# Optimization experiments

Hardware: AMD Instinct MI355X
Metric: run time of the kernel (lower is better)

Reference implementation:

```python
import jax, jax.numpy as jnp
import numpy as np

NT, NP, E, H, DIM = 100000, 50000, 800000, 128, 128


def _lin(key, fi, fo):
    k1, k2 = jax.random.split(key)
    w = jax.random.normal(k1, (fi, fo), jnp.float32) * 0.02
    b = jax.random.normal(k2, (fo,), jnp.float32) * 0.02
    return w, b


def _conv_params(key, d_src, d_dst, d_out):
    ks = jax.random.split(key, 5)
    Wq, bq = _lin(ks[0], d_dst, d_out)
    Wk, bk = _lin(ks[1], d_src, d_out)
    Wv, bv = _lin(ks[2], d_src, d_out)
    Ws, bs = _lin(ks[3], d_dst, d_out)
    Wb = jax.random.normal(ks[4], (3 * d_out, 1), jnp.float32) * 0.02
    return Wq, bq, Wk, bk, Wv, bv, Ws, bs, Wb


def setup_inputs() -> dict:
    key = jax.random.key(0)
    ks = jax.random.split(key, 12)
    inp = {}
    inp['x_token'] = jax.random.normal(ks[0], (NT, 1), jnp.float32)
    inp['x_phrase'] = jax.random.normal(ks[1], (NP, H), jnp.float32)
    inp['W_emb'], inp['b_emb'] = _lin(ks[2], 1, H)
    (inp['Wq_tp'], inp['bq_tp'], inp['Wk_tp'], inp['bk_tp'], inp['Wv_tp'],
     inp['bv_tp'], inp['Ws_tp'], inp['bs_tp'], inp['Wb_tp']) = _conv_params(ks[3], H, H, H)
    (inp['Wq_pt'], inp['bq_pt'], inp['Wk_pt'], inp['bk_pt'], inp['Wv_pt'],
     inp['bv_pt'], inp['Ws_pt'], inp['bs_pt'], inp['Wb_pt']) = _conv_params(ks[4], H, H, H)
    inp['W_head'], inp['b_head'] = _lin(ks[5], H, DIM)
    inp['src_tp'] = jax.random.randint(ks[6], (E,), 0, NT, jnp.int32)
    inp['dst_tp'] = jax.random.randint(ks[7], (E,), 0, NP, jnp.int32)
    inp['src_pt'] = jax.random.randint(ks[8], (E,), 0, NP, jnp.int32)
    inp['dst_pt'] = jax.random.randint(ks[9], (E,), 0, NT, jnp.int32)
    return inp


def _tconv(x_src, x_dst, src, dst, Wq, bq, Wk, bk, Wv, bv, Ws, bs, Wb):
    # PyG TransformerConv, heads=1, beta=True, eval mode (no dropout).
    n_dst = x_dst.shape[0]
    d = Wq.shape[1]
    q = x_dst @ Wq + bq          # [Ndst, d]
    k = x_src @ Wk + bk          # [Nsrc, d]
    v = x_src @ Wv + bv          # [Nsrc, d]
    scores = jnp.sum(q[dst] * k[src], axis=-1) / jnp.sqrt(jnp.float32(d))  # [E]
    m = jax.ops.segment_max(scores, dst, num_segments=n_dst)
    m = jnp.where(jnp.isfinite(m), m, 0.0)  # nodes with no in-edges
    e = jnp.exp(scores - m[dst])
    denom = jax.ops.segment_sum(e, dst, num_segments=n_dst)
    alpha = e / (denom[dst] + 1e-16)                       # segment softmax over dst
    out = jax.ops.segment_sum(alpha[:, None] * v[src], dst, num_segments=n_dst)
    skip = x_dst @ Ws + bs
    beta = jax.nn.sigmoid(jnp.concatenate([out, skip, out - skip], axis=-1) @ Wb)
    return beta * skip + (1.0 - beta) * out


def _forward(x_token, x_phrase, W_emb, b_emb,
             Wq_tp, bq_tp, Wk_tp, bk_tp, Wv_tp, bv_tp, Ws_tp, bs_tp, Wb_tp,
             Wq_pt, bq_pt, Wk_pt, bk_pt, Wv_pt, bv_pt, Ws_pt, bs_pt, Wb_pt,
             W_head, b_head, src_tp, dst_tp, src_pt, dst_pt):
    h_t = x_token @ W_emb + b_emb   # [NT, H]
    h_p = x_phrase                  # [NP, H]
    # conv1 (HeteroConv aggr='sum'; each node type has exactly one incoming edge type)
    p1 = _tconv(h_t, h_p, src_tp, dst_tp, Wq_tp, bq_tp, Wk_tp, bk_tp, Wv_tp, bv_tp, Ws_tp, bs_tp, Wb_tp)
    t1 = _tconv(h_p, h_t, src_pt, dst_pt, Wq_pt, bq_pt, Wk_pt, bk_pt, Wv_pt, bv_pt, Ws_pt, bs_pt, Wb_pt)
    p1 = jax.nn.leaky_relu(p1, 0.01)
    t1 = jax.nn.leaky_relu(t1, 0.01)
    # conv2 shares the SAME conv modules (same params). Only the token output is used downstream.
    t2 = _tconv(p1, t1, src_pt, dst_pt, Wq_pt, bq_pt, Wk_pt, bk_pt, Wv_pt, bv_pt, Ws_pt, bs_pt, Wb_pt)
    return t2 @ W_head + b_head     # [NT, DIM]


def reference(x_token, x_phrase, W_emb, b_emb, Wq_tp, bq_tp, Wk_tp, bk_tp, Wv_tp, bv_tp, Ws_tp, bs_tp, Wb_tp, Wq_pt, bq_pt, Wk_pt, bk_pt, Wv_pt, bv_pt, Ws_pt, bs_pt, Wb_pt, W_head, b_head, src_tp, dst_tp, src_pt, dst_pt):
    return _forward(x_token, x_phrase, W_emb, b_emb,
                    Wq_tp, bq_tp, Wk_tp, bk_tp, Wv_tp, bv_tp, Ws_tp, bs_tp, Wb_tp,
                    Wq_pt, bq_pt, Wk_pt, bk_pt, Wv_pt, bv_pt, Ws_pt, bs_pt, Wb_pt,
                    W_head, b_head, src_tp, dst_tp, src_pt, dst_pt)
```

## Files before the change

### kernel.cpp

```cpp
#include <hip/hip_runtime.h>
#include <math.h>

#define NT 100000
#define NP 50000
#define NE 800000
#define H 128
#define NB 196
#define BCAP 8192
#define SPAD 140

#define CDIV(a,b) (((a)+(b)-1)/(b))

typedef __attribute__((ext_vector_type(8))) short s16x8;
typedef __attribute__((ext_vector_type(4))) short s16x4;
typedef __attribute__((ext_vector_type(4))) unsigned short u16x4;
typedef __attribute__((ext_vector_type(4))) float f32x4;

static __device__ __forceinline__ float dot4(float4 a, float4 b){
  return a.x*b.x + a.y*b.y + a.z*b.z + a.w*b.w;
}
static __device__ __forceinline__ float b2f(unsigned short u){
  union { unsigned int i; float f; } c; c.i = ((unsigned int)u) << 16; return c.f;
}
static __device__ __forceinline__ unsigned short f2b(float f){
  union { float f; unsigned int i; } c; c.f = f;
  unsigned int x = c.i;
  unsigned int r = (x + 0x7fffu + ((x >> 16) & 1u)) >> 16;
  return (unsigned short)r;
}
static __device__ __forceinline__ float4 cvt4u(u16x4 h){
  return make_float4(b2f(h[0]), b2f(h[1]), b2f(h[2]), b2f(h[3]));
}

__global__ void kvec4(const float* __restrict__ e, const float* __restrict__ be,
    const float* W0, const float* bi0, float* u0, float* w0,
    const float* W1, const float* bi1, float* u1, float* w1,
    const float* W2, const float* bi2, float* u2, float* w2,
    const float* W3, const float* bi3, float* u3, float* w3){
  const float *W, *bi; float *u, *w;
  switch (blockIdx.x){
    case 0: W=W0; bi=bi0; u=u0; w=w0; break;
    case 1: W=W1; bi=bi1; u=u1; w=w1; break;
    case 2: W=W2; bi=bi2; u=u2; w=w2; break;
    default:W=W3; bi=bi3; u=u3; w=w3; break;
  }
  int j = threadIdx.x;
  float su = 0.f, sw = 0.f;
  for (int i = 0; i < H; ++i) {
    float wv = W[i*H + j];
    su += e[i]*wv;
    sw += be[i]*wv;
  }
  u[j] = su;
  w[j] = sw + bi[j];
}

__global__ void ksetup(const float* __restrict__ Wq, const float* __restrict__ Wk,
                       const float* __restrict__ bq, float* __restrict__ Wqk,
                       float* __restrict__ bqk){
  int i = blockIdx.x;
  int m = threadIdx.x;
  __shared__ float wqr[H];
  wqr[m] = Wq[i*H + m];
  __syncthreads();
  const float* wkr = Wk + m*H;
  float s = 0.f;
  for (int j = 0; j < H; ++j) s += wqr[j] * wkr[j];
  Wqk[i*H + m] = s;
  if (i == 0){
    float t = 0.f;
    for (int j = 0; j < H; ++j) t += bq[j] * wkr[j];
    bqk[m] = t;
  }
}
__global__ void kvqb(const float* __restrict__ Wq, const float* __restrict__ bq,
                     const float* __restrict__ bk, float* __restrict__ vqb,
                     float* __restrict__ c0){
  int i = threadIdx.x;
  float s = 0.f;
  for (int j = 0; j < H; ++j) s += Wq[i*H + j]*bk[j];
  vqb[i] = s;
  if (i == 0){
    float t = 0.f;
    for (int j = 0; j < H; ++j) t += bq[j]*bk[j];
    *c0 = t;
  }
}

__global__ void kprep(const float* W0, unsigned short* P0,
                      const float* W1, unsigned short* P1,
                      const float* W2, unsigned short* P2,
                      const float* W3, unsigned short* P3,
                      const float* W4, unsigned short* P4,
                      const float* W5, unsigned short* P5,
                      const float* W6, unsigned short* P6){
  const float* W; unsigned short* P;
  switch (blockIdx.x){
    case 0: W=W0; P=P0; break;
    case 1: W=W1; P=P1; break;
    case 2: W=W2; P=P2; break;
    case 3: W=W3; P=P3; break;
    case 4: W=W4; P=P4; break;
    case 5: W=W5; P=P5; break;
    default:W=W6; P=P6; break;
  }
  int tid = threadIdx.x;
  for (int it = 0; it < 16; ++it){
    int gid = it*256 + tid;
    int n  = gid & 127;
    int kg = gid >> 7;
    int k0 = kg*4;
    float w0 = W[(k0+0)*H + n];
    float w1 = W[(k0+1)*H + n];
    float w2 = W[(k0+2)*H + n];
    float w3 = W[(k0+3)*H + n];
    unsigned short h0=f2b(w0), h1=f2b(w1), h2=f2b(w2), h3=f2b(w3);
    s16x4 hv; hv[0]=(short)h0; hv[1]=(short)h1; hv[2]=(short)h2; hv[3]=(short)h3;
    s16x4 lv; lv[0]=(short)f2b(w0-b2f(h0)); lv[1]=(short)f2b(w1-b2f(h1));
              lv[2]=(short)f2b(w2-b2f(h2)); lv[3]=(short)f2b(w3-b2f(h3));
    int base = n*128 + (((kg>>1) ^ (n&15))<<3) + ((kg&1)<<2);
    *(s16x4*)(P + base) = hv;
    *(s16x4*)(P + 16384 + base) = lv;
  }
}

static __device__ __forceinline__ void stage_pre32_512(const unsigned short* __restrict__ Wpre,
    unsigned short* __restrict__ WH, int tid){
  const s16x8* src = (const s16x8*)Wpre;
  s16x8 tmp[4];
  #pragma unroll
  for (int it = 0; it < 4; ++it) tmp[it] = src[it*512 + tid];
  #pragma unroll
  for (int it = 0; it < 4; ++it) *(s16x8*)(WH + (it*512 + tid)*8) = tmp[it];
}

static __device__ __forceinline__ void mfma_passW2(const s16x8 AH[4], const s16x8 AL[4],
    const unsigned short* __restrict__ WH, int l15, int l4, f32x4 acc[8]){
  #pragma unroll
  for (int t = 0; t < 8; ++t){ acc[t][0]=0.f; acc[t][1]=0.f; acc[t][2]=0.f; acc[t][3]=0.f; }
  #pragma unroll
  for (int s = 0; s < 4; ++s){
    #pragma unroll
    for (int t = 0; t < 8; ++t){
      int n = t*16 + l15;
      int off = n*128 + (((s*4 + l4) ^ l15)<<3);
      s16x8 BH = *(const s16x8*)(WH + off);
      acc[t] = __builtin_amdgcn_mfma_f32_16x16x32_bf16(AH[s], BH, acc[t], 0,0,0);
      acc[t] = __builtin_amdgcn_mfma_f32_16x16x32_bf16(AL[s], BH, acc[t], 0,0,0);
    }
  }
}
static __device__ __forceinline__ void mfma_passW1(const s16x8 AH[4],
    const unsigned short* __restrict__ WH, int l15, int l4, f32x4 acc[8]){
  #pragma unroll
  for (int t = 0; t < 8; ++t){ acc[t][0]=0.f; acc[t][1]=0.f; acc[t][2]=0.f; acc[t][3]=0.f; }
  #pragma unroll
  for (int s = 0; s < 4; ++s){
    #pragma unroll
    for (int t = 0; t < 8; ++t){
      int n = t*16 + l15;
      int off = n*128 + (((s*4 + l4) ^ l15)<<3);
      s16x8 BH = *(const s16x8*)(WH + off);
      acc[t] = __builtin_amdgcn_mfma_f32_16x16x32_bf16(AH[s], BH, acc[t], 0,0,0);
    }
  }
}

static __device__ __forceinline__ void load_aw_f32(const float* __restrict__ X, int M,
    int rowb, int l15, int l4, s16x8 AH[4], s16x8 AL[4]){
  int row = rowb + l15;
  const float* xr = X + (size_t)row*H;
  bool ok = row < M;
  #pragma unroll
  for (int s = 0; s < 4; ++s){
    int kb = s*32 + l4*8;
    float4 f0 = ok ? *(const float4*)(xr+kb)   : make_float4(0.f,0.f,0.f,0.f);
    float4 f1 = ok ? *(const float4*)(xr+kb+4) : make_float4(0.f,0.f,0.f,0.f);
    float xs[8] = {f0.x,f0.y,f0.z,f0.w,f1.x,f1.y,f1.z,f1.w};
    s16x8 h, lo;
    #pragma unroll
    for (int e = 0; e < 8; ++e){
      unsigned short hh = f2b(xs[e]);
      h[e]  = (short)hh;
      lo[e] = (short)f2b(xs[e] - b2f(hh));
    }
    AH[s] = h; AL[s] = lo;
  }
}
static __device__ __forceinline__ void load_aw_bf16(const unsigned short* __restrict__ Xb, int M,
    int rowb, int l15, int l4, s16x8 AH[4]){
  int row = rowb + l15;
  const unsigned short* xr = Xb + (size_t)row*H;
  bool ok = row < M;
  #pragma unroll
  for (int s = 0; s < 4; ++s){
    s16x8 h = {0,0,0,0,0,0,0,0};
    if (ok) h = *(const s16x8*)(xr + s*32 + l4*8);
    AH[s] = h;
  }
}

static __device__ __forceinline__ void dots_epiW(const f32x4 (&acc)[8],
    const float* __restrict__ bias, const float* __restrict__ uvec,
    const float* __restrict__ wvec, float2* __restrict__ acout,
    int rowb, int M, int l15, int l4){
  float ub[8], wb[8], bb[8];
  #pragma unroll
  for (int t=0;t<8;++t){ ub[t]=uvec[t*16+l15]; wb[t]=wvec[t*16+l15]; bb[t]=bias[t*16+l15]; }
  #pragma unroll
  for (int r=0;r<4;++r){
    float pa=0.f, pc=0.f;
    #pragma unroll
    for (int t=0;t<8;++t){ float y=acc[t][r]+bb[t]; pa+=y*ub[t]; pc+=y*wb[t]; }
    #pragma unroll
    for (int o=1;o<16;o<<=1){ pa+=__shfl_xor(pa,o); pc+=__shfl_xor(pc,o); }
    int row = rowb + l4*4 + r;
    if (l15==0 && row<M) acout[row]=make_float2(pa,pc);
  }
}

static __device__ __forceinline__ void store_cw_bf16(unsigned short* __restrict__ Y,
    const f32x4 (&acc)[8], const float* __restrict__ bias,
    int rowb, int M, int l15, int l4){
  float bb[8];
  #pragma unroll
  for (int t=0;t<8;++t) bb[t]=bias[t*16+l15];
  #pragma unroll
  for (int r=0;r<4;++r){
    int row = rowb + l4*4 + r;
    if (row < M){
      unsigned short* dr = Y + (size_t)row*H;
      #pragma unroll
      for (int t=0;t<8;++t) dr[t*16+l15] = f2b(acc[t][r] + bb[t]);
    }
  }
}
static __device__ __forceinline__ void store_cw_f32(float* __restrict__ Y,
    const f32x4 (&acc)[8], const float* __restrict__ bias,
    int rowb, int M, int l15, int l4){
  float bb[8];
  #pragma unroll
  for (int t=0;t<8;++t) bb[t]=bias[t*16+l15];
  #pragma unroll
  for (int r=0;r<4;++r){
    int row = rowb + l4*4 + r;
    if (row < M){
      float* dr = Y + (size_t)row*H;
      #pragma unroll
      for (int t=0;t<8;++t) dr[t*16+l15] = acc[t][r] + bb[t];
    }
  }
}

__launch_bounds__(512)
__global__ void k_ph(const float* __restrict__ X, int M,
    const unsigned short* __restrict__ WqP, const float* __restrict__ bq,
    const float* __restrict__ uk, const float* __restrict__ wk, float2* __restrict__ ac1,
    const unsigned short* __restrict__ WsP, const float* __restrict__ bs, unsigned short* __restrict__ S1b,
    const unsigned short* __restrict__ WkP, const float* __restrict__ bk,
    const float* __restrict__ uq, const float* __restrict__ wq, float2* __restrict__ ac2,
    const unsigned short* __restrict__ WvP, const float* __restrict__ bv, unsigned short* __restrict__ Vb){
  __shared__ __align__(16) unsigned short WH[16384];
  int tid=threadIdx.x, lane=tid&63, w=tid>>6, l15=lane&15, l4=lane>>4;
  int rowb = blockIdx.x*128 + w*16;

  s16x8 AH[4], AL[4];
  load_aw_f32(X, M, rowb, l15, l4, AH, AL);

  f32x4 acc[8];
  stage_pre32_512(WqP, WH, tid); __syncthreads();
  mfma_passW2(AH, AL, WH, l15, l4, acc);
  __syncthreads();
  dots_epiW(acc, bq, uk, wk, ac1, rowb, M, l15, l4);

  stage_pre32_512(WsP, WH, tid); __syncthreads();
  mfma_passW2(AH, AL, WH, l15, l4, acc);
  __syncthreads();
  store_cw_bf16(S1b, acc, bs, rowb, M, l15, l4);

  stage_pre32_512(WkP, WH, tid); __syncthreads();
  mfma_passW2(AH, AL, WH, l15, l4, acc);
  __syncthreads();
  dots_epiW(acc, bk, uq, wq, ac2, rowb, M, l15, l4);

  stage_pre32_512(WvP, WH, tid); __syncthreads();
  mfma_passW2(AH, AL, WH, l15, l4, acc);
  store_cw_bf16(Vb, acc, bv, rowb, M, l15, l4);
}

__launch_bounds__(512)
__global__ void k_t3f(const unsigned short* __restrict__ T1b, int M,
    const unsigned short* __restrict__ PQK, const float* __restrict__ bqk,
    const float* __restrict__ vqb, const float* __restrict__ c0,
    const unsigned short* __restrict__ PS3, const float* __restrict__ bs3,
    const unsigned short* __restrict__ P1b,
    const int* __restrict__ rowptr, const int* __restrict__ deg,
    const int* __restrict__ srcs,
    const unsigned short* __restrict__ PV2, const float* __restrict__ bv,
    const float* __restrict__ Wb,
    const unsigned short* __restrict__ PHD, const float* __restrict__ bh,
    float* __restrict__ out){
  __shared__ __align__(16) unsigned short WH[16384];
  __shared__ __align__(16) unsigned short SLDS[128][SPAD];
  __shared__ float qbl[128];
  int tid=threadIdx.x, lane=tid&63, w=tid>>6, l15=lane&15, l4=lane>>4;
  int g = tid>>4, gl = tid&15;
  int row0 = blockIdx.x*128;
  int rowb = row0 + w*16;
  const float RS = 0.08838834764831845f;

  s16x8 AH[4];
  load_aw_bf16(T1b, M, rowb, l15, l4, AH);

  {
    float cc0 = *c0;
    float p = 0.f;
    #pragma unroll
    for (int s = 0; s < 4; ++s){
      #pragma unroll
      for (int e = 0; e < 8; ++e)
        p += b2f((unsigned short)AH[s][e]) * vqb[s*32 + l4*8 + e];
    }
    p += __shfl_xor(p, 16);
    p += __shfl_xor(p, 32);
    if (l4 == 0) qbl[w*16 + l15] = p + cc0;
  }

  stage_pre32_512(PQK, WH, tid);
  __syncthreads();
  {
    f32x4 acc[8];
    mfma_passW1(AH, WH, l15, l4, acc);
    float bb[8];
    #pragma unroll
    for (int t=0;t<8;++t) bb[t] = bqk[t*16+l15];
    #pragma unroll
    for (int r=0;r<4;++r){
      int rl = w*16 + l4*4 + r;
      #pragma unroll
      for (int t=0;t<8;++t) SLDS[rl][t*16+l15] = f2b(acc[t][r] + bb[t]);
    }
  }
  __syncthreads();

  stage_pre32_512(PS3, WH, tid);

  #pragma unroll
  for (int tk = 0; tk < 4; ++tk){
    int rl = g*4 + tk;
    int row = row0 + rl;
    if (row < M){
      float q[8];
      {
        s16x8 qh = *(const s16x8*)&SLDS[rl][gl*8];
        #pragma unroll
        for (int e = 0; e < 8; ++e) q[e] = b2f((unsigned short)qh[e]);
      }
      float qb = qbl[rl];
      int rp = rowptr[row], dg = deg[row];
      float d = 0.f;
      float acc8[8] = {0.f,0.f,0.f,0.f,0.f,0.f,0.f,0.f};
      for (int i0 = 0; i0 < dg; i0 += 16){
        int nrem = dg - i0; if (nrem > 16) nrem = 16;
        int mySp = (gl < nrem) ? srcs[rp + i0 + gl] : 0;
        int j = 0;
        for (; j+2 <= nrem; j += 2){
          int spA = __shfl(mySp, j, 16), spB = __shfl(mySp, j+1, 16);
          s16x8 hA = *(const s16x8*)(P1b + (size_t)spA*H + gl*8);
          s16x8 hB = *(const s16x8*)(P1b + (size_t)spB*H + gl*8);
          float pA[8], pB[8];
          float psA = 0.f, psB = 0.f;
          #pragma unroll
          for (int e = 0; e < 8; ++e){
            pA[e] = b2f((unsigned short)hA[e]);
            pB[e] = b2f((unsigned short)hB[e]);
            psA += q[e]*pA[e];
            psB += q[e]*pB[e];
          }
          #pragma unroll
          for (int off=1; off<16; off<<=1){ psA += __shfl_xor(psA,off); psB += __shfl_xor(psB,off); }
          float eA = __expf((psA + qb)*RS), eB = __expf((psB + qb)*RS);
          d += eA + eB;
          #pragma unroll
          for (int e = 0; e < 8; ++e) acc8[e] += eA*pA[e] + eB*pB[e];
        }
        if (j < nrem){
          int sp = __shfl(mySp, j, 16);
          s16x8 h = *(const s16x8*)(P1b + (size_t)sp*H + gl*8);
          float p[8];
          float ps = 0.f;
          #pragma unroll
          for (int e = 0; e < 8; ++e){ p[e] = b2f((unsigned short)h[e]); ps += q[e]*p[e]; }
          #pragma unroll
          for (int off=1; off<16; off<<=1) ps += __shfl_xor(ps,off);
          float ex = __expf((ps + qb)*RS);
          d += ex;
          #pragma unroll
          for (int e = 0; e < 8; ++e) acc8[e] += ex*p[e];
        }
      }
      float inv = 1.f/(d + 1e-16f);
      s16x8 hres;
      #pragma unroll
      for (int e = 0; e < 8; ++e) hres[e] = (short)f2b(acc8[e]*inv);
      *(s16x8*)&SLDS[rl][gl*8] = hres;
    } else {
      s16x8 z = {0,0,0,0,0,0,0,0};
      *(s16x8*)&SLDS[rl][gl*8] = z;
    }
  }
  __syncthreads();

  f32x4 skacc[8];
  mfma_passW1(AH, WH, l15, l4, skacc);
  s16x8 A2[4];
  {
    int rl = w*16 + l15;
    #pragma unroll
    for (int s = 0; s < 4; ++s)
      A2[s] = *(const s16x8*)&SLDS[rl][s*32 + l4*8];
  }
  __syncthreads();

  stage_pre32_512(PV2, WH, tid);
  __syncthreads();

  {
    f32x4 oacc[8];
    mfma_passW1(A2, WH, l15, l4, oacc);
    float bvv[8], bsv[8], wbA[8], wbB[8], wbC[8];
    #pragma unroll
    for (int t = 0; t < 8; ++t){
      int col = t*16 + l15;
      bvv[t] = bv[col]; bsv[t] = bs3[col];
      wbA[t] = Wb[col]; wbB[t] = Wb[H + col]; wbC[t] = Wb[2*H + col];
    }
    #pragma unroll
    for (int r = 0; r < 4; ++r){
      int rl = w*16 + l4*4 + r;
      int row = row0 + rl;
      bool ok = row < M;
      float bsc = (ok && deg[row] > 0) ? 1.f : 0.f;
      float o[8], sk[8];
      float part = 0.f;
      #pragma unroll
      for (int t = 0; t < 8; ++t){
        o[t]  = oacc[t][r] + bvv[t]*bsc;
        sk[t] = skacc[t][r] + bsv[t];
        part += o[t]*wbA[t] + sk[t]*wbB[t] + (o[t]-sk[t])*wbC[t];
      }
      #pragma unroll
      for (int of = 1; of < 16; of <<= 1) part += __shfl_xor(part, of);
      float beta = 1.f/(1.f + __expf(-part));
      #pragma unroll
      for (int t = 0; t < 8; ++t){
        float vv = beta*sk[t] + (1.f-beta)*o[t];
        SLDS[rl][t*16 + l15] = f2b(vv);
      }
    }
  }
  __syncthreads();

  s16x8 A3[4];
  {
    int rl = w*16 + l15;
    #pragma unroll
    for (int s = 0; s < 4; ++s)
      A3[s] = *(const s16x8*)&SLDS[rl][s*32 + l4*8];
  }
  stage_pre32_512(PHD, WH, tid);
  __syncthreads();

  f32x4 hacc[8];
  mfma_passW1(A3, WH, l15, l4, hacc);
  store_cw_f32(out, hacc, bh, rowb, M, l15, l4);
}

template<int GATHER>
__launch_bounds__(256)
__global__ void passA(const int* __restrict__ dst, const int* __restrict__ src,
                      const float* __restrict__ xv, int shift,
                      int* __restrict__ bcnt, int2* __restrict__ out, int n){
  __shared__ int hist[NB];
  __shared__ int base[NB];
  __shared__ int cur[NB];
  int tid = threadIdx.x;
  for (int i = tid; i < NB; i += 256){ hist[i]=0; cur[i]=0; }
  __syncthreads();
  int e0 = blockIdx.x*2048;
  int d[8], s[8];
  #pragma unroll
  for (int k = 0; k < 8; ++k){
    int i = e0 + k*256 + tid;
    if (i < n){ d[k] = dst[i]; s[k] = src[i]; }
    else d[k] = -1;
  }
  #pragma unroll
  for (int k = 0; k < 8; ++k)
    if (d[k] >= 0) atomicAdd(&hist[d[k]>>shift], 1);
  __syncthreads();
  for (int b = tid; b < NB; b += 256)
    base[b] = hist[b] ? atomicAdd(&bcnt[b], hist[b]) : 0;
  __syncthreads();
  #pragma unroll
  for (int k = 0; k < 8; ++k){
    if (d[k] >= 0){
      int b = d[k] >> shift;
      int loc = atomicAdd(&cur[b], 1);
      int2 rec;
      if constexpr (GATHER) rec.x = __float_as_int(xv[s[k]]);
      else                  rec.x = s[k];
      rec.y = d[k] - (b << shift);
      out[(size_t)b*BCAP + base[b] + loc] = rec;
    }
  }
}

__launch_bounds__(512)
__global__ void passB_ph(const int* __restrict__ bcnt, const int2* __restrict__ sorted,
                         const float2* __restrict__ ac, float2* __restrict__ dsv, int np){
  __shared__ float2 acl[256];
  __shared__ float accx[256];
  __shared__ float accy[256];
  int b = blockIdx.x, tid = threadIdx.x;
  int p0 = b*256;
  if (tid < 256){
    int p = p0 + tid;
    acl[tid] = (p < np) ? ac[p] : make_float2(0.f,0.f);
    accx[tid] = 0.f; accy[tid] = 0.f;
  }
  __syncthreads();
  int n = bcnt[b];
  const int2* e = sorted + (size_t)b*BCAP;
  const float RS = 0.08838834764831845f;
  for (int i = tid; i < n; i += 512){
    int2 ed = e[i];
    float x = __int_as_float(ed.x);
    float2 a = acl[ed.y];
    float ex = __expf((x*a.x + a.y)*RS);
    atomicAdd(&accx[ed.y], ex);
    atomicAdd(&accy[ed.y], ex*x);
  }
  __syncthreads();
  if (tid < 256){
    int p = p0 + tid;
    if (p < np) dsv[p] = make_float2(accx[tid], accy[tid]);
  }
}

__launch_bounds__(512)
__global__ void passB_tok(const int* __restrict__ bcnt, const int2* __restrict__ sorted,
                          int* __restrict__ rowptr, int* __restrict__ deg,
                          int* __restrict__ srcs, int ntok){
  __shared__ int cnt[512];
  __shared__ int scn[512];
  __shared__ int cur[512];
  int b = blockIdx.x, tid = threadIdx.x;
  cnt[tid] = 0; cur[tid] = 0;
  __syncthreads();
  int n = bcnt[b];
  const int2* e = sorted + (size_t)b*BCAP;
  for (int i = tid; i < n; i += 512) atomicAdd(&cnt[e[i].y], 1);
  __syncthreads();
  int myc = cnt[tid];
  scn[tid] = myc;
  __syncthreads();
  for (int off = 1; off < 512; off <<= 1){
    int u = (tid >= off) ? scn[tid-off] : 0;
    __syncthreads();
    scn[tid] += u;
    __syncthreads();
  }
  int excl = scn[tid] - myc;
  int tok = b*512 + tid;
  if (tok < ntok){ rowptr[tok] = b*BCAP + excl; deg[tok] = myc; }
  __syncthreads();
  cnt[tid] = excl;
  __syncthreads();
  for (int i = tid; i < n; i += 512){
    int2 ed = e[i];
    int pos = cnt[ed.y] + atomicAdd(&cur[ed.y], 1);
    srcs[(size_t)b*BCAP + pos] = ed.x;
  }
}

template<int OB>
static __device__ __forceinline__ void beta_combine(float4 o, float4 sk,
    const float* __restrict__ Wb, int lane, bool leaky, void* __restrict__ dstRow){
  float4 wb0 = *(const float4*)&Wb[lane*4];
  float4 wb1 = *(const float4*)&Wb[H   + lane*4];
  float4 wb2 = *(const float4*)&Wb[2*H + lane*4];
  float4 dv = make_float4(o.x-sk.x, o.y-sk.y, o.z-sk.z, o.w-sk.w);
  float part = dot4(o,wb0) + dot4(sk,wb1) + dot4(dv,wb2);
  #pragma unroll
  for (int off=1; off<32; off<<=1) part += __shfl_xor(part, off);
  float beta = 1.f/(1.f + __expf(-part));
  float4 r;
  r.x = beta*sk.x + (1.f-beta)*o.x;
  r.y = beta*sk.y + (1.f-beta)*o.y;
  r.z = beta*sk.z + (1.f-beta)*o.z;
  r.w = beta*sk.w + (1.f-beta)*o.w;
  if (leaky){
    r.x = r.x>0.f? r.x : 0.01f*r.x;
    r.y = r.y>0.f? r.y : 0.01f*r.y;
    r.z = r.z>0.f? r.z : 0.01f*r.z;
    r.w = r.w>0.f? r.w : 0.01f*r.w;
  }
  if constexpr (OB){
    ushort4 h; h.x=f2b(r.x); h.y=f2b(r.y); h.z=f2b(r.z); h.w=f2b(r.w);
    *(ushort4*)((unsigned short*)dstRow + lane*4) = h;
  } else {
    *(float4*)((float*)dstRow + lane*4) = r;
  }
}

static __device__ __forceinline__ void beta_combine16(const float o[8], const float sk[8],
    const float* __restrict__ Wb, int lane, bool leaky, unsigned short* __restrict__ dstRow){
  float part = 0.f;
  #pragma unroll
  for (int e = 0; e < 8; ++e){
    int col = lane*8 + e;
    part += o[e]*Wb[col] + sk[e]*Wb[H+col] + (o[e]-sk[e])*Wb[2*H+col];
  }
  #pragma unroll
  for (int off = 1; off < 16; off <<= 1) part += __shfl_xor(part, off);
  float beta = 1.f/(1.f + __expf(-part));
  s16x8 h;
  #pragma unroll
  for (int e = 0; e < 8; ++e){
    float r = beta*sk[e] + (1.f-beta)*o[e];
    if (leaky) r = r > 0.f ? r : 0.01f*r;
    h[e] = (short)f2b(r);
  }
  __builtin_nontemporal_store(h, (s16x8*)(dstRow + lane*8));
}

__global__ void kcomb1(const float2* __restrict__ dsv,
                       const float* __restrict__ uv, const float* __restrict__ wv,
                       const unsigned short* __restrict__ S, const float* __restrict__ Wb,
                       unsigned short* __restrict__ out, int n){
  int gid = (blockIdx.x*blockDim.x + threadIdx.x) >> 5;
  int lane = threadIdx.x & 31;
  if (gid >= n) return;
  float2 ds = dsv[gid];
  float d = ds.x, sv = ds.y;
  float inv = 1.f/(d + 1e-16f);
  float4 u4 = *(const float4*)&uv[lane*4];
  float4 w4 = *(const float4*)&wv[lane*4];
  float4 o = make_float4((sv*u4.x + d*w4.x)*inv, (sv*u4.y + d*w4.y)*inv,
                         (sv*u4.z + d*w4.z)*inv, (sv*u4.w + d*w4.w)*inv);
  u16x4 sh4 = __builtin_nontemporal_load((const u16x4*)(S + (size_t)gid*H + lane*4));
  float4 sk = cvt4u(sh4);
  beta_combine<1>(o, sk, Wb, lane, true, out + (size_t)gid*H);
}

__global__ void knode2(const float* __restrict__ x_tok, const float2* __restrict__ ac,
                       const unsigned short* __restrict__ Vb,
                       const int* __restrict__ rowptr, const int* __restrict__ deg,
                       const int* __restrict__ srcs,
                       const float* __restrict__ us, const float* __restrict__ ws,
                       const float* __restrict__ Wb, unsigned short* __restrict__ out, int n){
  int gid = (blockIdx.x*blockDim.x + threadIdx.x) >> 4;
  int lane = threadIdx.x & 15;
  if (gid >= n) return;
  float xt = x_tok[gid];
  int rp = rowptr[gid], dg = deg[gid];
  const float RS = 0.08838834764831845f;
  float d = 0.f;
  float acc[8] = {0.f,0.f,0.f,0.f,0.f,0.f,0.f,0.f};
  for (int i0 = 0; i0 < dg; i0 += 16){
    int nrem = dg - i0; if (nrem > 16) nrem = 16;
    int mySp = 0; float myE = 0.f;
    if (lane < nrem){
      mySp = srcs[rp + i0 + lane];
      float2 a = ac[mySp];
      myE = __expf((xt*a.x + a.y)*RS);
    }
    float cd = myE;
    #pragma unroll
    for (int of = 1; of < 16; of <<= 1) cd += __shfl_xor(cd, of);
    d += cd;
    int j = 0;
    for (; j+2 <= nrem; j += 2){
      int spA = __shfl(mySp, j, 16),  spB = __shfl(mySp, j+1, 16);
      float eA = __shfl(myE, j, 16),  eB = __shfl(myE, j+1, 16);
      s16x8 hA = *(const s16x8*)(Vb + (size_t)spA*H + lane*8);
      s16x8 hB = *(const s16x8*)(Vb + (size_t)spB*H + lane*8);
      #pragma unroll
      for (int e = 0; e < 8; ++e)
        acc[e] += eA*b2f((unsigned short)hA[e]) + eB*b2f((unsigned short)hB[e]);
    }
    if (j < nrem){
      int sp = __shfl(mySp, j, 16);
      float e0 = __shfl(myE, j, 16);
      s16x8 hv = *(const s16x8*)(Vb + (size_t)sp*H + lane*8);
      #pragma unroll
      for (int e = 0; e < 8; ++e) acc[e] += e0*b2f((unsigned short)hv[e]);
    }
  }
  float inv = 1.f/(d + 1e-16f);
  float o[8], sk[8];
  #pragma unroll
  for (int e = 0; e < 8; ++e){
    int col = lane*8 + e;
    o[e]  = acc[e]*inv;
    sk[e] = xt*us[col] + ws[col];
  }
  beta_combine16(o, sk, Wb, lane, true, out + (size_t)gid*H);
}

extern "C" void kernel_launch(void* const* d_in, const int* in_sizes, int n_in,
                              void* d_out, int out_size, void* d_ws, size_t ws_size,
                              hipStream_t stream){
  const float* x_token  = (const float*)d_in[0];
  const float* x_phrase = (const float*)d_in[1];
  const float* W_emb    = (const float*)d_in[2];
  const float* b_emb    = (const float*)d_in[3];
  const float* Wq_tp = (const float*)d_in[4];  const float* bq_tp = (const float*)d_in[5];
  const float* Wk_tp = (const float*)d_in[6];  const float* bk_tp = (const float*)d_in[7];
  const float* Wv_tp = (const float*)d_in[8];  const float* bv_tp = (const float*)d_in[9];
  const float* Ws_tp = (const float*)d_in[10]; const float* bs_tp = (const float*)d_in[11];
  const float* Wb_tp = (const float*)d_in[12];
  const float* Wq_pt = (const float*)d_in[13]; const float* bq_pt = (const float*)d_in[14];
  const float* Wk_pt = (const float*)d_in[15]; const float* bk_pt = (const float*)d_in[16];
  const float* Wv_pt = (const float*)d_in[17]; const float* bv_pt = (const float*)d_in[18];
  const float* Ws_pt = (const float*)d_in[19]; const float* bs_pt = (const float*)d_in[20];
  const float* Wb_pt = (const float*)d_in[21];
  const float* W_head = (const float*)d_in[22]; const float* b_head = (const float*)d_in[23];
  const int* src_tp = (const int*)d_in[24];
  const int* dst_tp = (const int*)d_in[25];
  const int* src_pt = (const int*)d_in[26];
  const int* dst_pt = (const int*)d_in[27];
  float* out = (float*)d_out;

  char* base = (char*)d_ws;
  size_t off = 0;
  auto AB = [&](size_t bytes)->void*{ void* p=(void*)(base+off); off += (bytes+15)&~(size_t)15; return p; };
  unsigned short* S1b = (unsigned short*)AB((size_t)NP*H*2);
  unsigned short* P1b = (unsigned short*)AB((size_t)NP*H*2);
  unsigned short* Vb  = (unsigned short*)AB((size_t)NP*H*2);
  unsigned short* T1b = (unsigned short*)AB((size_t)NT*H*2);
  float* Wqk = (float*)AB((size_t)H*H*4);
  float* bqk = (float*)AB((size_t)H*4);
  float* vqb = (float*)AB((size_t)H*4);
  float* c0  = (float*)AB(16);
  unsigned short* PQ1 = (unsigned short*)AB(32768*2);
  unsigned short* PS1 = (unsigned short*)AB(32768*2);
  unsigned short* PK2 = (unsigned short*)AB(32768*2);
  unsigned short* PV2 = (unsigned short*)AB(32768*2);
  unsigned short* PS3 = (unsigned short*)AB(32768*2);
  unsigned short* PHD = (unsigned short*)AB(32768*2);
  unsigned short* PQK = (unsigned short*)AB(32768*2);
  float* vecs = (float*)AB(8*H*4);
  float* uk1=vecs, *wk1=vecs+H, *uv1=vecs+2*H, *wv1=vecs+3*H;
  float* uq2=vecs+4*H, *wq2=vecs+5*H, *us2=vecs+6*H, *ws2=vecs+7*H;
  float2* ac1  = (float2*)AB((size_t)NP*8);
  float2* ac2  = (float2*)AB((size_t)NP*8);
  float2* dsv2 = (float2*)AB((size_t)NP*8);
  int2* sortedP = (int2*)AB((size_t)NB*BCAP*8);
  int2* sortedT = (int2*)AB((size_t)NB*BCAP*8);
  int*  srcsT   = (int*)AB((size_t)NB*BCAP*4);
  int* rowT = (int*)AB((size_t)NT*4);
  int* degT = (int*)AB((size_t)NT*4);
  int* bcnt = (int*)AB((size_t)2*NB*4);
  int* bcntP = bcnt, * bcntT = bcnt + NB;
  (void)ws_size; (void)in_sizes; (void)n_in; (void)out_size;

  const int gP = CDIV(NP,128), gT = CDIV(NT,128);
  const int nbA = CDIV(NE,2048);

  kvec4<<<4,H,0,stream>>>(W_emb, b_emb,
      Wk_tp, bk_tp, uk1, wk1,
      Wv_tp, bv_tp, uv1, wv1,
      Wq_pt, bq_pt, uq2, wq2,
      Ws_pt, bs_pt, us2, ws2);
  ksetup<<<H,H,0,stream>>>(Wq_pt, Wk_pt, bq_pt, Wqk, bqk);
  kvqb<<<1,H,0,stream>>>(Wq_pt, bq_pt, bk_pt, vqb, c0);
  kprep<<<7,256,0,stream>>>(Wq_tp, PQ1, Ws_tp, PS1, Wk_pt, PK2, Wv_pt, PV2,
                            Ws_pt, PS3, W_head, PHD, Wqk, PQK);

  (void)hipMemsetAsync(bcnt, 0, (size_t)2*NB*4, stream);
  passA<1><<<nbA,256,0,stream>>>(dst_tp, src_tp, x_token, 8, bcntP, sortedP, NE);
  passA<0><<<nbA,256,0,stream>>>(dst_pt, src_pt, nullptr, 9, bcntT, sortedT, NE);
  passB_tok<<<NB,512,0,stream>>>(bcntT, sortedT, rowT, degT, srcsT, NT);

  k_ph<<<gP,512,0,stream>>>(x_phrase, NP,
      PQ1, bq_tp, uk1, wk1, ac1,
      PS1, bs_tp, S1b,
      PK2, bk_pt, uq2, wq2, ac2,
      PV2, bv_pt, Vb);

  passB_ph<<<NB,512,0,stream>>>(bcntP, sortedP, ac1, dsv2, NP);
  kcomb1<<<CDIV(NP*32,256),256,0,stream>>>(dsv2, uv1, wv1, S1b, Wb_tp, P1b, NP);

  knode2<<<CDIV(NT*16,256),256,0,stream>>>(x_token, ac2, Vb, rowT, degT, srcsT,
                                           us2, ws2, Wb_pt, T1b, NT);

  k_t3f<<<gT,512,0,stream>>>(T1b, NT,
      PQK, bqk, vqb, c0,
      PS3, bs_pt,
      P1b, rowT, degT, srcsT,
      PV2, bv_pt, Wb_pt,
      PHD, b_head, out);
}
```

Measured before the change: 239.8 us.

## Stage weights in K-halves to halve LDS footprint in fused token kernel

The fused final-layer kernel now stages each 128x128 bf16 weight matrix into LDS as two K-halves of 8192 elements instead of all at once. The LDS weight buffer and the SLDS padding both shrink, and the prepacked layout and swizzle change to a per-half 64-wide XOR pattern to match. The goal is to cut shared memory per block so more blocks fit per CU, which should help hide the latency of the irregular gather loop. In exchange each GEMM needs extra __syncthreads and restage steps, and the smaller SPAD may add bank conflicts.

```diff
diff --git a/kernel.cpp b/kernel.cpp
--- a/kernel.cpp
+++ b/kernel.cpp
@@ -7,7 +7,7 @@
 #define H 128
 #define NB 196
 #define BCAP 8192
-#define SPAD 140
+#define SPAD 132
 
 #define CDIV(a,b) (((a)+(b)-1)/(b))
 
@@ -118,7 +118,9 @@
     s16x4 hv; hv[0]=(short)h0; hv[1]=(short)h1; hv[2]=(short)h2; hv[3]=(short)h3;
     s16x4 lv; lv[0]=(short)f2b(w0-b2f(h0)); lv[1]=(short)f2b(w1-b2f(h1));
               lv[2]=(short)f2b(w2-b2f(h2)); lv[3]=(short)f2b(w3-b2f(h3));
-    int base = n*128 + (((kg>>1) ^ (n&15))<<3) + ((kg&1)<<2);
+    int h = kg >> 4;
+    int c = (kg >> 1) & 7;
+    int base = h*8192 + n*64 + ((c ^ (n & 7))<<3) + ((kg & 1)<<2);
     *(s16x4*)(P + base) = hv;
     *(s16x4*)(P + 16384 + base) = lv;
   }
@@ -133,6 +135,14 @@
   #pragma unroll
   for (int it = 0; it < 4; ++it) *(s16x8*)(WH + (it*512 + tid)*8) = tmp[it];
 }
+static __device__ __forceinline__ void stage_half_512(const unsigned short* __restrict__ Wpre,
+    int half, unsigned short* __restrict__ WH, int tid){
+  const s16x8* src = (const s16x8*)(Wpre + half*8192);
+  s16x8 a = src[tid];
+  s16x8 b = src[512 + tid];
+  *(s16x8*)(WH + tid*8) = a;
+  *(s16x8*)(WH + 4096 + tid*8) = b;
+}
 
 static __device__ __forceinline__ void mfma_passW2(const s16x8 AH[4], const s16x8 AL[4],
     const unsigned short* __restrict__ WH, int l15, int l4, f32x4 acc[8]){
@@ -143,27 +153,29 @@
     #pragma unroll
     for (int t = 0; t < 8; ++t){
       int n = t*16 + l15;
-      int off = n*128 + (((s*4 + l4) ^ l15)<<3);
+      int off = (s>>1)*8192 + n*64 + ((((s&1)*4 + l4) ^ (l15 & 7))<<3);
       s16x8 BH = *(const s16x8*)(WH + off);
       acc[t] = __builtin_amdgcn_mfma_f32_16x16x32_bf16(AH[s], BH, acc[t], 0,0,0);
       acc[t] = __builtin_amdgcn_mfma_f32_16x16x32_bf16(AL[s], BH, acc[t], 0,0,0);
     }
   }
 }
-static __device__ __forceinline__ void mfma_passW1(const s16x8 AH[4],
-    const unsigned short* __restrict__ WH, int l15, int l4, f32x4 acc[8]){
-  #pragma unroll
-  for (int t = 0; t < 8; ++t){ acc[t][0]=0.f; acc[t][1]=0.f; acc[t][2]=0.f; acc[t][3]=0.f; }
-  #pragma unroll
-  for (int s = 0; s < 4; ++s){
+static __device__ __forceinline__ void mfma_half(const s16x8 A[4],
+    const unsigned short* __restrict__ WH, int h, int l15, int l4, f32x4 acc[8]){
+  #pragma unroll
+  for (int sl = 0; sl < 2; ++sl){
     #pragma unroll
     for (int t = 0; t < 8; ++t){
       int n = t*16 + l15;
-      int off = n*128 + (((s*4 + l4) ^ l15)<<3);
+      int off = n*64 + (((sl*4 + l4) ^ (l15 & 7))<<3);
       s16x8 BH = *(const s16x8*)(WH + off);
-      acc[t] = __builtin_amdgcn_mfma_f32_16x16x32_bf16(AH[s], BH, acc[t], 0,0,0);
-    }
-  }
+      acc[t] = __builtin_amdgcn_mfma_f32_16x16x32_bf16(A[h*2+sl], BH, acc[t], 0,0,0);
+    }
+  }
+}
+static __device__ __forceinline__ void zero8(f32x4 acc[8]){
+  #pragma unroll
+  for (int t = 0; t < 8; ++t){ acc[t][0]=0.f; acc[t][1]=0.f; acc[t][2]=0.f; acc[t][3]=0.f; }
 }
 
 static __device__ __forceinline__ void load_aw_f32(const float* __restrict__ X, int M,
@@ -300,7 +312,7 @@
     const float* __restrict__ Wb,
     const unsigned short* __restrict__ PHD, const float* __restrict__ bh,
     float* __restrict__ out){
-  __shared__ __align__(16) unsigned short WH[16384];
+  __shared__ __align__(16) unsigned short WH[8192];
   __shared__ __align__(16) unsigned short SLDS[128][SPAD];
   __shared__ float qbl[128];
   int tid=threadIdx.x, lane=tid&63, w=tid>>6, l15=lane&15, l4=lane>>4;
@@ -326,11 +338,16 @@
     if (l4 == 0) qbl[w*16 + l15] = p + cc0;
   }
 
-  stage_pre32_512(PQK, WH, tid);
+  stage_half_512(PQK, 0, WH, tid);
   __syncthreads();
   {
     f32x4 acc[8];
-    mfma_passW1(AH, WH, l15, l4, acc);
+    zero8(acc);
+    mfma_half(AH, WH, 0, l15, l4, acc);
+    __syncthreads();
+    stage_half_512(PQK, 1, WH, tid);
+    __syncthreads();
+    mfma_half(AH, WH, 1, l15, l4, acc);
     float bb[8];
     #pragma unroll
     for (int t=0;t<8;++t) bb[t] = bqk[t*16+l15];
@@ -343,7 +360,7 @@
   }
   __syncthreads();
 
-  stage_pre32_512(PS3, WH, tid);
+  stage_half_512(PS3, 0, WH, tid);
 
   #pragma unroll
   for (int tk = 0; tk < 4; ++tk){
@@ -412,7 +429,8 @@
   __syncthreads();
 
   f32x4 skacc[8];
-  mfma_passW1(AH, WH, l15, l4, skacc);
+  zero8(skacc);
+  mfma_half(AH, WH, 0, l15, l4, skacc);
   s16x8 A2[4];
   {
     int rl = w*16 + l15;
@@ -421,13 +439,21 @@
       A2[s] = *(const s16x8*)&SLDS[rl][s*32 + l4*8];
   }
   __syncthreads();
-
-  stage_pre32_512(PV2, WH, tid);
-  __syncthreads();
-
+  stage_half_512(PS3, 1, WH, tid);
+  __syncthreads();
+  mfma_half(AH, WH, 1, l15, l4, skacc);
+  __syncthreads();
+
+  stage_half_512(PV2, 0, WH, tid);
+  __syncthreads();
+  f32x4 oacc[8];
+  zero8(oacc);
+  mfma_half(A2, WH, 0, l15, l4, oacc);
+  __syncthreads();
+  stage_half_512(PV2, 1, WH, tid);
+  __syncthreads();
+  mfma_half(A2, WH, 1, l15, l4, oacc);
   {
-    f32x4 oacc[8];
-    mfma_passW1(A2, WH, l15, l4, oacc);
     float bvv[8], bsv[8], wbA[8], wbB[8], wbC[8];
     #pragma unroll
     for (int t = 0; t < 8; ++t){
@@ -468,11 +494,15 @@
     for (int s = 0; s < 4; ++s)
       A3[s] = *(const s16x8*)&SLDS[rl][s*32 + l4*8];
   }
-  stage_pre32_512(PHD, WH, tid);
-  __syncthreads();
-
+  stage_half_512(PHD, 0, WH, tid);
+  __syncthreads();
   f32x4 hacc[8];
-  mfma_passW1(A3, WH, l15, l4, hacc);
+  zero8(hacc);
+  mfma_half(A3, WH, 0, l15, l4, hacc);
+  __syncthreads();
+  stage_half_512(PHD, 1, WH, tid);
+  __syncthreads();
+  mfma_half(A3, WH, 1, l15, l4, hacc);
   store_cw_f32(out, hacc, bh, rowb, M, l15, l4);
 }
 
```

Measured after the change: 241.4 us. About the same (+0.6%).
